# Performance work log

Measured on AMD Instinct MI355X. Metric: run time of the kernel, lower is better.

## Reference

```python
import math
import jax, jax.numpy as jnp
import numpy as np

B, D, COND, H, K, L, BOUND = 262144, 16, 8, 128, 10, 4, 1.0
D2 = math.ceil(D / 2)          # second split (spline-transformed channels) = 8
D1 = D - D2                    # passthrough channels = 8
DOUT = (3 * K + 1) * D2        # subnet output = 248
PMIN = 1e-3                    # BIN_WIDTH_MIN == BIN_HEIGHT_MIN == DELTA_MIN


def setup_inputs() -> dict:
    key = jax.random.key(0)
    ks = jax.random.split(key, 8)
    x = jax.random.normal(ks[0], (B, D), dtype=jnp.float32)
    c = jax.random.normal(ks[1], (B, COND), dtype=jnp.float32)
    din1 = D1 + COND
    W1s = jax.random.normal(ks[2], (L, din1, H), dtype=jnp.float32) * 0.1
    b1s = jnp.zeros((L, H), dtype=jnp.float32)
    Whs = jax.random.normal(ks[3], (L, H, H), dtype=jnp.float32) * 0.1
    bhs = jnp.zeros((L, H), dtype=jnp.float32)
    Wos = jax.random.normal(ks[4], (L, H, DOUT), dtype=jnp.float32) * 0.1
    bos = jnp.zeros((L, DOUT), dtype=jnp.float32)
    rng = np.random.default_rng(0)  # permutation_seed = 0
    perms = jnp.asarray(np.stack([rng.permutation(D) for _ in range(L)]), dtype=jnp.int32)
    return {"x": x, "c": c, "W1s": W1s, "b1s": b1s, "Whs": Whs, "bhs": bhs,
            "Wos": Wos, "bos": bos, "perms": perms}


def _softmax_with_min(t, m):
    return m + (1.0 - m * t.shape[-1]) * jax.nn.softmax(t, axis=-1)


def _unpack_theta(theta):
    # theta: [B, D2, 3K+1]
    bw_u, bh_u, ks_u = theta[..., :K], theta[..., K:2 * K], theta[..., 2 * K:]
    bin_w = 2.0 * BOUND * _softmax_with_min(bw_u, PMIN)
    bin_h = 2.0 * BOUND * _softmax_with_min(bh_u, PMIN)
    slopes = PMIN + (1.0 - PMIN) * jax.nn.softplus(ks_u) / math.log(2.0)
    pad = ((0, 0), (0, 0), (1, 0))
    x_knots = jnp.pad(jnp.cumsum(bin_w, axis=-1), pad) - BOUND
    y_knots = jnp.pad(jnp.cumsum(bin_h, axis=-1), pad) - BOUND
    return x_knots, y_knots, bin_w, bin_h, slopes


def _spline_fwd(x2, x_knots, y_knots, bin_w, bin_h, slopes):
    # x2: [B, D2]; knots: [B, D2, K+1]; widths/heights: [B, D2, K]; slopes: [B, D2, K+1]
    bin_idx = jnp.sum(x_knots < x2[..., None], axis=-1) - 1  # searchsorted(left) - 1
    in_bounds = (bin_idx >= 0) & (bin_idx < K)
    ci = jnp.clip(bin_idx, 0, K - 1)
    g = lambda t, i: jnp.take_along_axis(t, i[..., None], axis=-1)[..., 0]
    x1, y1 = g(x_knots, ci), g(y_knots, ci)
    xw, yw = g(bin_w, ci), g(bin_h, ci)
    d1, d2 = g(slopes, ci), g(slopes, ci + 1)
    # safe x so rational-quadratic never produces nan for masked-out lanes
    xs = jnp.where(in_bounds, x2, x1 + 0.5 * xw)
    s = yw / xw
    eta = (xs - x1) / xw
    rev_eta = 1.0 - eta
    err = eta * rev_eta
    y_denom = s + (d1 + d2 - 2.0 * s) * err
    y_rq = y1 + yw * (s * eta ** 2 + d1 * err) / y_denom
    jac_num = s ** 2 * (d2 * eta ** 2 + 2.0 * s * err + d1 * rev_eta ** 2)
    log_jac = jnp.log(jac_num) - 2.0 * jnp.log(y_denom)
    # out-of-bounds: linear extrapolation through the outermost knots
    xl, xr = x_knots[..., 0], x_knots[..., -1]
    yb, yt = y_knots[..., 0], y_knots[..., -1]
    y_lin = (yt - yb) / (xr - xl) * (x2 - xl) + yb
    yx = jnp.where(in_bounds, y_rq, y_lin)
    log_jac = jnp.where(in_bounds, log_jac, 0.0)
    return yx, jnp.sum(log_jac, axis=-1)


def _flow_forward(x, c, W1s, b1s, Whs, bhs, Wos, bos, perms):
    log_jac_det = jnp.zeros((x.shape[0],), dtype=x.dtype)
    for i in range(L):
        x1, x2 = x[:, :D1], x[:, D1:]
        h = jax.nn.relu(jnp.concatenate([x1, c], axis=1) @ W1s[i] + b1s[i])
        h = jax.nn.relu(h @ Whs[i] + bhs[i])
        theta = (h @ Wos[i] + bos[i]).reshape(-1, D2, 3 * K + 1)
        x_knots, y_knots, bin_w, bin_h, slopes = _unpack_theta(theta)
        y2, ljd = _spline_fwd(x2, x_knots, y_knots, bin_w, bin_h, slopes)
        log_jac_det = log_jac_det + ljd
        x_out = jnp.concatenate([x1, y2], axis=1)
        x = jnp.take(x_out, perms[i], axis=1)  # x @ channel_perm.T
    return x, log_jac_det


def reference(x, c, W1s, b1s, Whs, bhs, Wos, bos, perms):
    return _flow_forward(x, c, W1s, b1s, Whs, bhs, Wos, bos, perms)
```

## Files before the change

### kernel.cpp

```cpp
#include <hip/hip_runtime.h>

#define B_N   262144
#define PMIN_F 0.001f
#define LOG2E 1.44269504088896340736f
#define LN2   0.69314718055994530942f

typedef _Float16 half4v __attribute__((ext_vector_type(4)));
typedef _Float16 half8  __attribute__((ext_vector_type(8)));
typedef float    floatx4 __attribute__((ext_vector_type(4)));

__device__ __forceinline__ float fexp2(float x) { return __builtin_amdgcn_exp2f(x); }
__device__ __forceinline__ float flog2(float x) { return __builtin_amdgcn_logf(x); }
__device__ __forceinline__ float frcp (float x) { return __builtin_amdgcn_rcpf(x); }

__global__ __launch_bounds__(64) void prep_kernel(
    const float* __restrict__ W1s, const float* __restrict__ b1s,
    const float* __restrict__ Whs, const float* __restrict__ Wos,
    _Float16* __restrict__ ws)
{
    const int bid   = blockIdx.x;
    const int layer = bid / 104;
    const int r     = bid % 104;
    const int lane  = threadIdx.x;
    const int kg    = lane >> 4;
    const int c     = lane & 15;

    half8 v;
    if (r < 8) {
        const int nt = r, n = nt * 16 + c;
        const float* W1 = W1s + layer * 16 * 128;
        const float* b1 = b1s + layer * 128;
        #pragma unroll
        for (int j = 0; j < 8; ++j) {
            const int k = kg * 8 + j;
            v[j] = (k < 16) ? (_Float16)W1[k * 128 + n]
                 : (k == 16) ? (_Float16)b1[n] : (_Float16)0.f;
        }
    } else if (r < 40) {
        const int f = r - 8, nt = f >> 2, ks = f & 3, n = nt * 16 + c;
        const float* Wh = Whs + layer * 128 * 128;
        #pragma unroll
        for (int j = 0; j < 8; ++j) {
            const int k = ks * 32 + kg * 8 + j;
            v[j] = (_Float16)Wh[k * 128 + n];
        }
    } else {
        const int f = r - 40, nt = f >> 2, ks = f & 3, n = nt * 16 + c;
        const int dd = n >> 5, cc = n & 31;
        const float* Wo = Wos + layer * 128 * 248;
        #pragma unroll
        for (int j = 0; j < 8; ++j) {
            const int k = ks * 32 + kg * 8 + j;
            v[j] = (cc < 31) ? (_Float16)Wo[k * 248 + dd * 31 + cc] : (_Float16)0.f;
        }
    }
    *(half8*)(ws + (size_t)bid * 512 + lane * 8) = v;
}

__global__ __launch_bounds__(64, 3) void flow_mfma(
    const float* __restrict__ x_in,
    const float* __restrict__ c_in,
    const float* __restrict__ bhs,
    const float* __restrict__ bos,
    const int*   __restrict__ perms,
    const _Float16* __restrict__ wsW,
    float* __restrict__ out)
{
    __shared__ __align__(16) float    xls[2][256];
    __shared__ __align__(16) _Float16 R[2][2112];

    const int lane = threadIdx.x;
    const int q    = lane >> 4;
    const int m    = lane & 15;
    const long long row0 = (long long)blockIdx.x * 32;

    {
        const float4* xp = (const float4*)(x_in + row0 * 16);
        *(float4*)&xls[0][lane * 4] = xp[lane];
        *(float4*)&xls[1][lane * 4] = xp[lane + 64];
    }

    half8 a1c[2];
    #pragma unroll
    for (int t2 = 0; t2 < 2; ++t2) {
        #pragma unroll
        for (int j = 0; j < 8; ++j) a1c[t2][j] = (_Float16)0.f;
        if (q == 1) {
            const float4* cp = (const float4*)(c_in + (row0 + t2 * 16 + m) * 8);
            const float4 c0 = cp[0], c1 = cp[1];
            a1c[t2][0] = (_Float16)c0.x; a1c[t2][1] = (_Float16)c0.y;
            a1c[t2][2] = (_Float16)c0.z; a1c[t2][3] = (_Float16)c0.w;
            a1c[t2][4] = (_Float16)c1.x; a1c[t2][5] = (_Float16)c1.y;
            a1c[t2][6] = (_Float16)c1.z; a1c[t2][7] = (_Float16)c1.w;
        } else if (q == 2) {
            a1c[t2][0] = (_Float16)1.f;
        }
    }
    __syncthreads();

    float ljrow[2] = {0.f, 0.f};

    for (int l = 0; l < 4; ++l) {
        const _Float16* wsl = wsW + (size_t)l * 104 * 512;
        const float* bh = bhs + l * 128;
        const float* bo = bos + l * 248;

        half8 a1[2];
        #pragma unroll
        for (int t2 = 0; t2 < 2; ++t2) {
            a1[t2] = a1c[t2];
            if (q == 0) {
                const float4 lo = *(const float4*)&xls[t2][m * 16];
                const float4 hi = *(const float4*)&xls[t2][m * 16 + 4];
                a1[t2][0] = (_Float16)lo.x; a1[t2][1] = (_Float16)lo.y;
                a1[t2][2] = (_Float16)lo.z; a1[t2][3] = (_Float16)lo.w;
                a1[t2][4] = (_Float16)hi.x; a1[t2][5] = (_Float16)hi.y;
                a1[t2][6] = (_Float16)hi.z; a1[t2][7] = (_Float16)hi.w;
            }
        }
        #pragma unroll
        for (int g = 0; g < 2; ++g) {
            const floatx4 z = {0.f, 0.f, 0.f, 0.f};
            floatx4 acc0[4], acc1[4];
            #pragma unroll
            for (int nt = 0; nt < 4; ++nt) {
                const half8 b = *(const half8*)(wsl + (g * 4 + nt) * 512 + lane * 8);
                acc0[nt] = __builtin_amdgcn_mfma_f32_16x16x32_f16(a1[0], b, z, 0, 0, 0);
                acc1[nt] = __builtin_amdgcn_mfma_f32_16x16x32_f16(a1[1], b, z, 0, 0, 0);
            }
            #pragma unroll
            for (int nt = 0; nt < 4; ++nt)
                #pragma unroll
                for (int reg = 0; reg < 4; ++reg) {
                    R[0][(q * 4 + reg) * 132 + (g * 4 + nt) * 16 + m] = (_Float16)fmaxf(acc0[nt][reg], 0.f);
                    R[1][(q * 4 + reg) * 132 + (g * 4 + nt) * 16 + m] = (_Float16)fmaxf(acc1[nt][reg], 0.f);
                }
        }
        __syncthreads();

        half8 a2[2][4];
        #pragma unroll
        for (int t2 = 0; t2 < 2; ++t2)
            #pragma unroll
            for (int ks = 0; ks < 4; ++ks) {
                const half4v lo = *(const half4v*)&R[t2][m * 132 + ks * 32 + q * 8];
                const half4v hi = *(const half4v*)&R[t2][m * 132 + ks * 32 + q * 8 + 4];
                a2[t2][ks] = __builtin_shufflevector(lo, hi, 0, 1, 2, 3, 4, 5, 6, 7);
            }
        __syncthreads();
        #pragma unroll
        for (int g = 0; g < 2; ++g) {
            floatx4 acc0[4], acc1[4];
            #pragma unroll
            for (int nt = 0; nt < 4; ++nt) {
                const float bb = bh[(g * 4 + nt) * 16 + m];
                acc0[nt][0] = bb; acc0[nt][1] = bb; acc0[nt][2] = bb; acc0[nt][3] = bb;
                acc1[nt] = acc0[nt];
            }
            #pragma unroll
            for (int ks = 0; ks < 4; ++ks)
                #pragma unroll
                for (int nt = 0; nt < 4; ++nt) {
                    const half8 b = *(const half8*)(wsl + (8 + (g * 4 + nt) * 4 + ks) * 512 + lane * 8);
                    acc0[nt] = __builtin_amdgcn_mfma_f32_16x16x32_f16(a2[0][ks], b, acc0[nt], 0, 0, 0);
                    acc1[nt] = __builtin_amdgcn_mfma_f32_16x16x32_f16(a2[1][ks], b, acc1[nt], 0, 0, 0);
                }
            #pragma unroll
            for (int nt = 0; nt < 4; ++nt)
                #pragma unroll
                for (int reg = 0; reg < 4; ++reg) {
                    R[0][(q * 4 + reg) * 132 + (g * 4 + nt) * 16 + m] = (_Float16)fmaxf(acc0[nt][reg], 0.f);
                    R[1][(q * 4 + reg) * 132 + (g * 4 + nt) * 16 + m] = (_Float16)fmaxf(acc1[nt][reg], 0.f);
                }
        }
        __syncthreads();

        half8 a3[2][4];
        #pragma unroll
        for (int t2 = 0; t2 < 2; ++t2)
            #pragma unroll
            for (int ks = 0; ks < 4; ++ks) {
                const half4v lo = *(const half4v*)&R[t2][m * 132 + ks * 32 + q * 8];
                const half4v hi = *(const half4v*)&R[t2][m * 132 + ks * 32 + q * 8 + 4];
                a3[t2][ks] = __builtin_shufflevector(lo, hi, 0, 1, 2, 3, 4, 5, 6, 7);
            }
        __syncthreads();

        #pragma unroll
        for (int hf = 0; hf < 2; ++hf) {
            #pragma unroll
            for (int g = 0; g < 2; ++g) {
                floatx4 acc0[4], acc1[4];
                #pragma unroll
                for (int nt4 = 0; nt4 < 4; ++nt4) {
                    const int nt = hf * 8 + g * 4 + nt4;
                    const float bb = ((nt & 1) && m == 15) ? 0.f
                                   : bo[(nt >> 1) * 31 + (nt & 1) * 16 + m];
                    acc0[nt4][0] = bb; acc0[nt4][1] = bb; acc0[nt4][2] = bb; acc0[nt4][3] = bb;
                    acc1[nt4] = acc0[nt4];
                }
                #pragma unroll
                for (int ks = 0; ks < 4; ++ks)
                    #pragma unroll
                    for (int nt4 = 0; nt4 < 4; ++nt4) {
                        const int nt = hf * 8 + g * 4 + nt4;
                        const half8 b = *(const half8*)(wsl + (40 + nt * 4 + ks) * 512 + lane * 8);
                        acc0[nt4] = __builtin_amdgcn_mfma_f32_16x16x32_f16(a3[0][ks], b, acc0[nt4], 0, 0, 0);
                        acc1[nt4] = __builtin_amdgcn_mfma_f32_16x16x32_f16(a3[1][ks], b, acc1[nt4], 0, 0, 0);
                    }
                #pragma unroll
                for (int nt4 = 0; nt4 < 4; ++nt4)
                    #pragma unroll
                    for (int reg = 0; reg < 4; ++reg) {
                        R[0][(q * 4 + reg) * 132 + (g * 4 + nt4) * 16 + m] = (_Float16)acc0[nt4][reg];
                        R[1][(q * 4 + reg) * 132 + (g * 4 + nt4) * 16 + m] = (_Float16)acc1[nt4][reg];
                    }
            }
            __syncthreads();

            #pragma unroll
            for (int itp = 0; itp < 2; ++itp) {
                const int t2   = itp;
                const int row  = lane >> 2;
                const int dloc = lane & 3;
                const int d    = hf * 4 + dloc;
                const int base = row * 132 + dloc * 32;

                const half4v v0 = *(const half4v*)&R[t2][base];
                const half4v v1 = *(const half4v*)&R[t2][base + 4];
                const half4v v2 = *(const half4v*)&R[t2][base + 8];
                const half4v v3 = *(const half4v*)&R[t2][base + 12];
                const half4v v4 = *(const half4v*)&R[t2][base + 16];
                const float x2 = xls[t2][row * 16 + 8 + d];

                float tw[10];
                tw[0]=(float)v0[0]; tw[1]=(float)v0[1]; tw[2]=(float)v0[2]; tw[3]=(float)v0[3];
                tw[4]=(float)v1[0]; tw[5]=(float)v1[1]; tw[6]=(float)v1[2]; tw[7]=(float)v1[3];
                tw[8]=(float)v2[0]; tw[9]=(float)v2[1];
                float m1 = tw[0];
                #pragma unroll
                for (int i = 1; i < 10; ++i) m1 = fmaxf(m1, tw[i]);
                float se = 0.f;
                #pragma unroll
                for (int i = 0; i < 10; ++i) { tw[i] = fexp2((tw[i] - m1) * LOG2E); se += tw[i]; }
                const float inv198 = 1.98f * frcp(se);

                int cnt = 0;
                {
                    float run = -1.f;
                    cnt += (run < x2) ? 1 : 0;
                    #pragma unroll
                    for (int i = 0; i < 10; ++i) {
                        run = run + fmaf(tw[i], inv198, 0.002f);
                        cnt += (run < x2) ? 1 : 0;
                    }
                }
                const int bidx = cnt - 1;
                const bool inb = (bidx >= 0) && (bidx < 10);
                const int ci = bidx < 0 ? 0 : (bidx > 9 ? 9 : bidx);

                float xlo = -1.f, xhi = 0.f, rx;
                {
                    float run = -1.f;
                    #pragma unroll
                    for (int i = 0; i < 10; ++i) {
                        const bool pick = (i == ci);
                        xlo = pick ? run : xlo;
                        run = run + fmaf(tw[i], inv198, 0.002f);
                        xhi = pick ? run : xhi;
                    }
                    rx = run;
                }

                float hm;
                {
                    const float h0=(float)v2[2], h1=(float)v2[3];
                    const float h2=(float)v3[0], h3=(float)v3[1];
                    const float h4=(float)v3[2], h5=(float)v3[3];
                    const float h6=(float)v4[0], h7=(float)v4[1];
                    const float h8=(float)v4[2], h9=(float)v4[3];
                    hm = fmaxf(fmaxf(fmaxf(h0,h1),fmaxf(h2,h3)),
                               fmaxf(fmaxf(h4,h5),fmaxf(fmaxf(h6,h7),fmaxf(h8,h9))));
                }
                float seh = 0.f;
                {
                    seh += fexp2(((float)v2[2] - hm) * LOG2E);
                    seh += fexp2(((float)v2[3] - hm) * LOG2E);
                    seh += fexp2(((float)v3[0] - hm) * LOG2E);
                    seh += fexp2(((float)v3[1] - hm) * LOG2E);
                    seh += fexp2(((float)v3[2] - hm) * LOG2E);
                    seh += fexp2(((float)v3[3] - hm) * LOG2E);
                    seh += fexp2(((float)v4[0] - hm) * LOG2E);
                    seh += fexp2(((float)v4[1] - hm) * LOG2E);
                    seh += fexp2(((float)v4[2] - hm) * LOG2E);
                    seh += fexp2(((float)v4[3] - hm) * LOG2E);
                }
                const float invh = 1.98f * frcp(seh);
                float ylo = -1.f, yhi = 0.f, ry;
                {
                    float run = -1.f;
                    #pragma unroll
                    for (int i = 0; i < 10; ++i) {
                        const float hv = (i < 2) ? (float)v2[2 + i]
                                      : (i < 6) ? (float)v3[i - 2]
                                                : (float)v4[i - 6];
                        const float e = fexp2((hv - hm) * LOG2E);
                        const bool pick = (i == ci);
                        ylo = pick ? run : ylo;
                        run = run + fmaf(e, invh, 0.002f);
                        yhi = pick ? run : yhi;
                    }
                    ry = run;
                }

                const float xw = xhi - xlo, yw = yhi - ylo;

                const float u1 = (float)R[t2][base + 20 + ci];
                const float u2 = (float)R[t2][base + 21 + ci];
                const float t1 = u1 * LOG2E;
                const float t2s = u2 * LOG2E;
                const float dd1 = PMIN_F + 0.999f * ((t1  > 15.f) ? t1  : flog2(1.f + fexp2(t1)));
                const float dd2 = PMIN_F + 0.999f * ((t2s > 15.f) ? t2s : flog2(1.f + fexp2(t2s)));

                const float xs  = inb ? x2 : (xlo + 0.5f * xw);
                const float rxw = frcp(xw);
                const float s   = yw * rxw;
                const float eta = (xs - xlo) * rxw;
                const float rev = 1.f - eta;
                const float er  = eta * rev;
                const float dn  = s + (dd1 + dd2 - 2.f * s) * er;
                const float yrq = ylo + yw * (s * eta * eta + dd1 * er) * frcp(dn);
                const float jn  = s * s * (dd2 * eta * eta + 2.f * s * er + dd1 * rev * rev);
                const float ljx = LN2 * (flog2(jn) - 2.f * flog2(dn));
                const float ylin = (ry + 1.f) * frcp(rx + 1.f) * (x2 + 1.f) - 1.f;

                xls[t2][row * 16 + 8 + d] = inb ? yrq : ylin;

                float lj = inb ? ljx : 0.f;
                lj += __shfl_xor(lj, 1);
                lj += __shfl_xor(lj, 2);
                ljrow[t2] += lj;
            }
            __syncthreads();
        }

        {
            const int4 pv = ((const int4*)(perms + l * 16))[lane & 3];
            const int mm = lane >> 2;
            const float a0 = xls[0][mm * 16 + pv.x];
            const float a1v = xls[0][mm * 16 + pv.y];
            const float a2v = xls[0][mm * 16 + pv.z];
            const float a3v = xls[0][mm * 16 + pv.w];
            const float b0 = xls[1][mm * 16 + pv.x];
            const float b1v = xls[1][mm * 16 + pv.y];
            const float b2 = xls[1][mm * 16 + pv.z];
            const float b3 = xls[1][mm * 16 + pv.w];
            __syncthreads();
            *(float4*)&xls[0][lane * 4] = make_float4(a0, a1v, a2v, a3v);
            *(float4*)&xls[1][lane * 4] = make_float4(b0, b1v, b2, b3);
        }
        __syncthreads();
    }

    #pragma unroll
    for (int t2 = 0; t2 < 2; ++t2) {
        const float4 vo = *(const float4*)&xls[t2][lane * 4];
        ((float4*)(out + (row0 + t2 * 16) * 16))[lane] = vo;
    }
    #pragma unroll
    for (int t2 = 0; t2 < 2; ++t2) {
        const float v = __shfl(ljrow[t2], (lane & 15) * 4);
        if (lane < 16)
            out[(size_t)B_N * 16 + row0 + t2 * 16 + lane] = v;
    }
}

extern "C" void kernel_launch(void* const* d_in, const int* in_sizes, int n_in,
                              void* d_out, int out_size, void* d_ws, size_t ws_size,
                              hipStream_t stream) {
    const float* x     = (const float*)d_in[0];
    const float* c     = (const float*)d_in[1];
    const float* W1s   = (const float*)d_in[2];
    const float* b1s   = (const float*)d_in[3];
    const float* Whs   = (const float*)d_in[4];
    const float* bhs   = (const float*)d_in[5];
    const float* Wos   = (const float*)d_in[6];
    const float* bos   = (const float*)d_in[7];
    const int*   perms = (const int*)d_in[8];
    float* out = (float*)d_out;
    _Float16* ws = (_Float16*)d_ws;

    prep_kernel<<<dim3(416), dim3(64), 0, stream>>>(W1s, b1s, Whs, Wos, ws);
    flow_mfma<<<dim3(B_N / 32), dim3(64), 0, stream>>>(
        x, c, bhs, bos, perms, ws, out);
}
```

Before: 301.5 us.

## Restructure spline stage into four quarters, keep theta in fp32, drop barriers

The output-layer GEMM and spline evaluation now run in four quarters of two channels each instead of two halves of four. Every lane handles one (tile, row, channel) spline per quarter, so both row tiles are processed at once rather than in a per-tile loop. Theta is staged in shared memory as fp32 instead of fp16, and the per-layer log-jacobian reduction shrinks to a single shuffle at the end. Many __syncthreads are removed because the workgroup is a single wavefront, relying on lockstep execution within the wave, which risks LDS read/write hazards if the compiler reorders accesses.

```diff
diff --git a/kernel.cpp b/kernel.cpp
--- a/kernel.cpp
+++ b/kernel.cpp
@@ -67,7 +67,7 @@
     float* __restrict__ out)
 {
     __shared__ __align__(16) float    xls[2][256];
-    __shared__ __align__(16) _Float16 R[2][2112];
+    __shared__ __align__(16) _Float16 R[2][2176];
 
     const int lane = threadIdx.x;
     const int q    = lane >> 4;
@@ -96,9 +96,12 @@
             a1c[t2][0] = (_Float16)1.f;
         }
     }
-    __syncthreads();
-
-    float ljrow[2] = {0.f, 0.f};
+
+    const int sp_t2  = lane >> 5;
+    const int sp_row = (lane & 31) >> 1;
+    const int sp_dl  = lane & 1;
+
+    float ljacc = 0.f;
 
     for (int l = 0; l < 4; ++l) {
         const _Float16* wsl = wsW + (size_t)l * 104 * 512;
@@ -136,7 +139,6 @@
                     R[1][(q * 4 + reg) * 132 + (g * 4 + nt) * 16 + m] = (_Float16)fmaxf(acc1[nt][reg], 0.f);
                 }
         }
-        __syncthreads();
 
         half8 a2[2][4];
         #pragma unroll
@@ -147,7 +149,6 @@
                 const half4v hi = *(const half4v*)&R[t2][m * 132 + ks * 32 + q * 8 + 4];
                 a2[t2][ks] = __builtin_shufflevector(lo, hi, 0, 1, 2, 3, 4, 5, 6, 7);
             }
-        __syncthreads();
         #pragma unroll
         for (int g = 0; g < 2; ++g) {
             floatx4 acc0[4], acc1[4];
@@ -173,7 +174,6 @@
                     R[1][(q * 4 + reg) * 132 + (g * 4 + nt) * 16 + m] = (_Float16)fmaxf(acc1[nt][reg], 0.f);
                 }
         }
-        __syncthreads();
 
         half8 a3[2][4];
         #pragma unroll
@@ -186,57 +186,54 @@
             }
         __syncthreads();
 
-        #pragma unroll
-        for (int hf = 0; hf < 2; ++hf) {
-            #pragma unroll
-            for (int g = 0; g < 2; ++g) {
+        float* Rf0 = (float*)&R[0][0];
+        float* Rf1 = (float*)&R[1][0];
+
+        #pragma unroll
+        for (int qd = 0; qd < 4; ++qd) {
+            {
                 floatx4 acc0[4], acc1[4];
                 #pragma unroll
-                for (int nt4 = 0; nt4 < 4; ++nt4) {
-                    const int nt = hf * 8 + g * 4 + nt4;
-                    const float bb = ((nt & 1) && m == 15) ? 0.f
-                                   : bo[(nt >> 1) * 31 + (nt & 1) * 16 + m];
-                    acc0[nt4][0] = bb; acc0[nt4][1] = bb; acc0[nt4][2] = bb; acc0[nt4][3] = bb;
-                    acc1[nt4] = acc0[nt4];
+                for (int j = 0; j < 4; ++j) {
+                    const int n = qd * 64 + j * 16 + m;
+                    const int cc = n & 31;
+                    const float bb = (cc < 31) ? bo[(n >> 5) * 31 + cc] : 0.f;
+                    acc0[j][0] = bb; acc0[j][1] = bb; acc0[j][2] = bb; acc0[j][3] = bb;
+                    acc1[j] = acc0[j];
                 }
                 #pragma unroll
                 for (int ks = 0; ks < 4; ++ks)
                     #pragma unroll
-                    for (int nt4 = 0; nt4 < 4; ++nt4) {
-                        const int nt = hf * 8 + g * 4 + nt4;
+                    for (int j = 0; j < 4; ++j) {
+                        const int nt = qd * 4 + j;
                         const half8 b = *(const half8*)(wsl + (40 + nt * 4 + ks) * 512 + lane * 8);
-                        acc0[nt4] = __builtin_amdgcn_mfma_f32_16x16x32_f16(a3[0][ks], b, acc0[nt4], 0, 0, 0);
-                        acc1[nt4] = __builtin_amdgcn_mfma_f32_16x16x32_f16(a3[1][ks], b, acc1[nt4], 0, 0, 0);
-                    }
-                #pragma unroll
-                for (int nt4 = 0; nt4 < 4; ++nt4)
+                        acc0[j] = __builtin_amdgcn_mfma_f32_16x16x32_f16(a3[0][ks], b, acc0[j], 0, 0, 0);
+                        acc1[j] = __builtin_amdgcn_mfma_f32_16x16x32_f16(a3[1][ks], b, acc1[j], 0, 0, 0);
+                    }
+                #pragma unroll
+                for (int j = 0; j < 4; ++j) {
+                    const int off = (j >> 1) * 32 + (j & 1) * 16 + m;
                     #pragma unroll
                     for (int reg = 0; reg < 4; ++reg) {
-                        R[0][(q * 4 + reg) * 132 + (g * 4 + nt4) * 16 + m] = (_Float16)acc0[nt4][reg];
-                        R[1][(q * 4 + reg) * 132 + (g * 4 + nt4) * 16 + m] = (_Float16)acc1[nt4][reg];
-                    }
-            }
-            __syncthreads();
-
-            #pragma unroll
-            for (int itp = 0; itp < 2; ++itp) {
-                const int t2   = itp;
-                const int row  = lane >> 2;
-                const int dloc = lane & 3;
-                const int d    = hf * 4 + dloc;
-                const int base = row * 132 + dloc * 32;
-
-                const half4v v0 = *(const half4v*)&R[t2][base];
-                const half4v v1 = *(const half4v*)&R[t2][base + 4];
-                const half4v v2 = *(const half4v*)&R[t2][base + 8];
-                const half4v v3 = *(const half4v*)&R[t2][base + 12];
-                const half4v v4 = *(const half4v*)&R[t2][base + 16];
-                const float x2 = xls[t2][row * 16 + 8 + d];
-
-                float tw[10];
-                tw[0]=(float)v0[0]; tw[1]=(float)v0[1]; tw[2]=(float)v0[2]; tw[3]=(float)v0[3];
-                tw[4]=(float)v1[0]; tw[5]=(float)v1[1]; tw[6]=(float)v1[2]; tw[7]=(float)v1[3];
-                tw[8]=(float)v2[0]; tw[9]=(float)v2[1];
+                        Rf0[(q * 4 + reg) * 68 + off] = acc0[j][reg];
+                        Rf1[(q * 4 + reg) * 68 + off] = acc1[j][reg];
+                    }
+                }
+            }
+
+            {
+                const int d    = qd * 2 + sp_dl;
+                const int base = sp_row * 68 + sp_dl * 32;
+                const float* Rf = sp_t2 ? Rf1 : Rf0;
+
+                const float4 v0 = *(const float4*)&Rf[base];
+                const float4 v1 = *(const float4*)&Rf[base + 4];
+                const float4 v2 = *(const float4*)&Rf[base + 8];
+                const float4 v3 = *(const float4*)&Rf[base + 12];
+                const float4 v4 = *(const float4*)&Rf[base + 16];
+                const float x2 = xls[sp_t2][sp_row * 16 + 8 + d];
+
+                float tw[10] = {v0.x, v0.y, v0.z, v0.w, v1.x, v1.y, v1.z, v1.w, v2.x, v2.y};
                 float m1 = tw[0];
                 #pragma unroll
                 for (int i = 1; i < 10; ++i) m1 = fmaxf(m1, tw[i]);
@@ -272,42 +269,22 @@
                     rx = run;
                 }
 
-                float hm;
-                {
-                    const float h0=(float)v2[2], h1=(float)v2[3];
-                    const float h2=(float)v3[0], h3=(float)v3[1];
-                    const float h4=(float)v3[2], h5=(float)v3[3];
-                    const float h6=(float)v4[0], h7=(float)v4[1];
-                    const float h8=(float)v4[2], h9=(float)v4[3];
-                    hm = fmaxf(fmaxf(fmaxf(h0,h1),fmaxf(h2,h3)),
-                               fmaxf(fmaxf(h4,h5),fmaxf(fmaxf(h6,h7),fmaxf(h8,h9))));
-                }
+                float hh[10] = {v2.z, v2.w, v3.x, v3.y, v3.z, v3.w, v4.x, v4.y, v4.z, v4.w};
+                float hm = hh[0];
+                #pragma unroll
+                for (int i = 1; i < 10; ++i) hm = fmaxf(hm, hh[i]);
                 float seh = 0.f;
-                {
-                    seh += fexp2(((float)v2[2] - hm) * LOG2E);
-                    seh += fexp2(((float)v2[3] - hm) * LOG2E);
-                    seh += fexp2(((float)v3[0] - hm) * LOG2E);
-                    seh += fexp2(((float)v3[1] - hm) * LOG2E);
-                    seh += fexp2(((float)v3[2] - hm) * LOG2E);
-                    seh += fexp2(((float)v3[3] - hm) * LOG2E);
-                    seh += fexp2(((float)v4[0] - hm) * LOG2E);
-                    seh += fexp2(((float)v4[1] - hm) * LOG2E);
-                    seh += fexp2(((float)v4[2] - hm) * LOG2E);
-                    seh += fexp2(((float)v4[3] - hm) * LOG2E);
-                }
+                #pragma unroll
+                for (int i = 0; i < 10; ++i) { hh[i] = fexp2((hh[i] - hm) * LOG2E); seh += hh[i]; }
                 const float invh = 1.98f * frcp(seh);
                 float ylo = -1.f, yhi = 0.f, ry;
                 {
                     float run = -1.f;
                     #pragma unroll
                     for (int i = 0; i < 10; ++i) {
-                        const float hv = (i < 2) ? (float)v2[2 + i]
-                                      : (i < 6) ? (float)v3[i - 2]
-                                                : (float)v4[i - 6];
-                        const float e = fexp2((hv - hm) * LOG2E);
                         const bool pick = (i == ci);
                         ylo = pick ? run : ylo;
-                        run = run + fmaf(e, invh, 0.002f);
+                        run = run + fmaf(hh[i], invh, 0.002f);
                         yhi = pick ? run : yhi;
                     }
                     ry = run;
@@ -315,8 +292,8 @@
 
                 const float xw = xhi - xlo, yw = yhi - ylo;
 
-                const float u1 = (float)R[t2][base + 20 + ci];
-                const float u2 = (float)R[t2][base + 21 + ci];
+                const float u1 = Rf[base + 20 + ci];
+                const float u2 = Rf[base + 21 + ci];
                 const float t1 = u1 * LOG2E;
                 const float t2s = u2 * LOG2E;
                 const float dd1 = PMIN_F + 0.999f * ((t1  > 15.f) ? t1  : flog2(1.f + fexp2(t1)));
@@ -334,14 +311,9 @@
                 const float ljx = LN2 * (flog2(jn) - 2.f * flog2(dn));
                 const float ylin = (ry + 1.f) * frcp(rx + 1.f) * (x2 + 1.f) - 1.f;
 
-                xls[t2][row * 16 + 8 + d] = inb ? yrq : ylin;
-
-                float lj = inb ? ljx : 0.f;
-                lj += __shfl_xor(lj, 1);
-                lj += __shfl_xor(lj, 2);
-                ljrow[t2] += lj;
-            }
-            __syncthreads();
+                xls[sp_t2][sp_row * 16 + 8 + d] = inb ? yrq : ylin;
+                ljacc += inb ? ljx : 0.f;
+            }
         }
 
         {
@@ -355,7 +327,6 @@
             const float b1v = xls[1][mm * 16 + pv.y];
             const float b2 = xls[1][mm * 16 + pv.z];
             const float b3 = xls[1][mm * 16 + pv.w];
-            __syncthreads();
             *(float4*)&xls[0][lane * 4] = make_float4(a0, a1v, a2v, a3v);
             *(float4*)&xls[1][lane * 4] = make_float4(b0, b1v, b2, b3);
         }
@@ -367,11 +338,10 @@
         const float4 vo = *(const float4*)&xls[t2][lane * 4];
         ((float4*)(out + (row0 + t2 * 16) * 16))[lane] = vo;
     }
-    #pragma unroll
-    for (int t2 = 0; t2 < 2; ++t2) {
-        const float v = __shfl(ljrow[t2], (lane & 15) * 4);
-        if (lane < 16)
-            out[(size_t)B_N * 16 + row0 + t2 * 16 + lane] = v;
+    {
+        const float ljs = ljacc + __shfl_xor(ljacc, 1);
+        if ((lane & 1) == 0)
+            out[(size_t)B_N * 16 + row0 + sp_t2 * 16 + sp_row] = ljs;
     }
 }
 
```

Result: faster. 281.0 us (-6.8%).
